# Performance work log

Measured on AMD Instinct MI355X. Metric: run time of the kernel, lower is better.

## Reference

```python
import jax, jax.numpy as jnp
import numpy as np

NEG_SLOPE = 0.2
EPS = 1e-5


def gatv2_conv(x, src, dst, Wl, Wr, att, bias, n_nodes):
    # x: [N, F_in]; Wl, Wr: [F_in, H*C]; att: [H, C]; bias: [C]
    H, C = att.shape
    xl = (x @ Wl).reshape(n_nodes, H, C)
    xr = (x @ Wr).reshape(n_nodes, H, C)
    # edge-wise GATv2 score: att . leaky_relu(xl[src] + xr[dst])
    xls = xl[src]                                   # [E, H, C]
    e = jax.nn.leaky_relu(xls + xr[dst], negative_slope=NEG_SLOPE)
    score = jnp.einsum('ehc,hc->eh', e, att)        # [E, H]
    # segment softmax over incoming edges of each dst node
    m = jax.ops.segment_max(score, dst, num_segments=n_nodes)
    expv = jnp.exp(score - m[dst])
    denom = jax.ops.segment_sum(expv, dst, num_segments=n_nodes)
    alpha = expv / denom[dst]                       # [E, H]
    out = jax.ops.segment_sum(xls * alpha[:, :, None], dst, num_segments=n_nodes)  # [N, H, C]
    return out.mean(axis=1) + bias                  # concat=False -> mean heads


def batchnorm(x, gamma, beta):
    mu = x.mean(axis=0)
    var = x.var(axis=0)
    return (x - mu) * jax.lax.rsqrt(var + EPS) * gamma + beta


def setup_inputs() -> dict:
    key = jax.random.key(0)
    ks = jax.random.split(key, 16)
    N, E = 50000, 400000
    F_in, Hd, H, Z = 32, 64, 4, 64

    def glorot(k, shape):
        fan_in, fan_out = shape[0], shape[-1]
        s = float(np.sqrt(6.0 / (fan_in + fan_out)))
        return jax.random.uniform(k, shape, jnp.float32, -s, s)

    return {
        'x': jax.random.normal(ks[0], (N, F_in), jnp.float32),
        'edge_index': jax.random.randint(ks[1], (2, E), 0, N, jnp.int64),
        'l': jax.random.uniform(ks[2], (N,), jnp.float32),
        'Wl1': glorot(ks[3], (F_in, H * Hd)),
        'Wr1': glorot(ks[4], (F_in, H * Hd)),
        'att1': glorot(ks[5], (H, Hd)),
        'b1': jnp.zeros((Hd,), jnp.float32),
        'g1': jnp.ones((Hd,), jnp.float32),
        'be1': jnp.zeros((Hd,), jnp.float32),
        'Wl2': glorot(ks[6], (Hd + 1, H * Hd)),
        'Wr2': glorot(ks[7], (Hd + 1, H * Hd)),
        'att2': glorot(ks[8], (H, Hd)),
        'b2': jnp.zeros((Hd,), jnp.float32),
        'g2': jnp.ones((Hd,), jnp.float32),
        'be2': jnp.zeros((Hd,), jnp.float32),
        'Wlin': glorot(ks[9], (Hd, 2 * Z)),
        'blin': jnp.zeros((2 * Z,), jnp.float32),
    }


def reference(x, edge_index, l, Wl1, Wr1, att1, b1, g1, be1,
              Wl2, Wr2, att2, b2, g2, be2, Wlin, blin):
    N = x.shape[0]
    loop = jnp.arange(N, dtype=edge_index.dtype)
    src = jnp.concatenate([edge_index[0], loop])  # add self-loops (PyG default)
    dst = jnp.concatenate([edge_index[1], loop])

    h = gatv2_conv(x, src, dst, Wl1, Wr1, att1, b1, N)
    h = jax.nn.relu(batchnorm(h, g1, be1))
    h = jnp.concatenate([h, l[:, None]], axis=-1)
    h = gatv2_conv(h, src, dst, Wl2, Wr2, att2, b2, N)
    h = jax.nn.relu(batchnorm(h, g2, be2))
    h = h @ Wlin + blin
    return h.mean(axis=0)  # [2*z_dim]
```

## Files before the change

kernel.cpp:

```cpp
#include <hip/hip_runtime.h>
#include <hip/hip_bf16.h>

typedef __hip_bfloat16 bf16;
typedef unsigned short u16;
typedef unsigned char u8;

#define NEG 0.2f
#define BN_EPS 1e-5f
#define SLOTS 64

typedef __attribute__((ext_vector_type(8))) short bfrag;
typedef __attribute__((ext_vector_type(4))) float ffrag;
typedef __attribute__((ext_vector_type(2))) float f32x2;

__device__ __forceinline__ float u2f(u16 u) { return __uint_as_float(((unsigned)u) << 16); }
__device__ __forceinline__ float lo2f(unsigned u) { return __uint_as_float(u << 16); }
__device__ __forceinline__ float hi2f(unsigned u) { return __uint_as_float(u & 0xffff0000u); }
__device__ __forceinline__ u16 f2b(float f) { bf16 t = __float2bfloat16(f); return *(u16*)&t; }
__device__ __forceinline__ float leaky(float x) { return fmaxf(x, NEG * x); }

__device__ __forceinline__ unsigned pk_fp8(float f0, float f1, float f2, float f3) {
    unsigned w = 0;
    w = __builtin_amdgcn_cvt_pk_fp8_f32(f0, f1, w, false);
    w = __builtin_amdgcn_cvt_pk_fp8_f32(f2, f3, w, true);
    return w;
}

__device__ __forceinline__ void prep_body(const float* __restrict__ Wl,
                                          const float* __restrict__ Wr,
                                          u16* __restrict__ Wbf, int K, int idx) {
    const int l = idx & 63, n = (idx >> 6) & 31, s = idx >> 11;
    const int col = n * 16 + (l & 15);
    const int kbase = s * 32 + ((l >> 4) << 3);
    const float* __restrict__ W = (col < 256) ? (Wl + col) : (Wr + col - 256);
    u16 v[8];
    #pragma unroll
    for (int j = 0; j < 8; ++j) {
        const int k = kbase + j;
        v[j] = (k < K) ? f2b(W[(size_t)k * 256]) : (u16)0;
    }
    ushort4* d = reinterpret_cast<ushort4*>(Wbf + (size_t)idx * 8);
    d[0] = make_ushort4(v[0], v[1], v[2], v[3]);
    d[1] = make_ushort4(v[4], v[5], v[6], v[7]);
}

__global__ __launch_bounds__(256) void k_misc(
    const float* __restrict__ Wl1, const float* __restrict__ Wr1,
    const float* __restrict__ Wl2, const float* __restrict__ Wr2,
    u16* __restrict__ WbfA, u16* __restrict__ WbfB,
    int* __restrict__ deg, int* __restrict__ scalars, int N) {
    const int b = blockIdx.x;
    if (b < 8) {
        prep_body(Wl1, Wr1, WbfA, 32, b * 256 + threadIdx.x);
    } else if (b < 32) {
        prep_body(Wl2, Wr2, WbfB, 65, (b - 8) * 256 + threadIdx.x);
    } else if (b == 32) {
        scalars[threadIdx.x] = 0;
        scalars[threadIdx.x + 256] = 0;
    } else {
        const int i = (b - 33) * 256 + (int)threadIdx.x;
        if (i < (N + 3) / 4)
            *reinterpret_cast<int4*>(deg + i * 4) = make_int4(0, 0, 0, 0);
    }
}

template <int KSTEPS, int STAGE>
__device__ __forceinline__ void gemm_body(
    int bid,
    const float* __restrict__ Xf,
    const u16* __restrict__ hagg,
    const float* __restrict__ sums, const float* __restrict__ sumsq,
    const float* __restrict__ g, const float* __restrict__ be,
    const float* __restrict__ lf,
    const u16* __restrict__ Wbf,
    u8* __restrict__ xl, u8* __restrict__ xr, int N) {

    __shared__ u16 sA[32 * 104];
    __shared__ u16 sC[32 * 512];
    __shared__ float ssc[64], ssh[64];

    const int tid = threadIdx.x;
    const int row0 = bid * 32;

    if (STAGE == 1) {
        if (tid < 64) {
            const float invN = 1.0f / (float)N;
            const float mu = sums[tid] * invN;
            const float var = sumsq[tid] * invN - mu * mu;
            const float sc = rsqrtf(var + BN_EPS) * g[tid];
            ssc[tid] = sc;
            ssh[tid] = be[tid] - mu * sc;
        }
        __syncthreads();
        for (int idx = tid; idx < 32 * 12; idx += 256) {
            const int r = idx / 12, c0 = (idx % 12) * 8;
            const int rr = row0 + r;
            u16 o[8] = {0, 0, 0, 0, 0, 0, 0, 0};
            if (rr < N) {
                if (c0 < 64) {
                    const uint4 hv = *reinterpret_cast<const uint4*>(hagg + (size_t)rr * 64 + c0);
                    const float f[8] = {lo2f(hv.x), hi2f(hv.x), lo2f(hv.y), hi2f(hv.y),
                                        lo2f(hv.z), hi2f(hv.z), lo2f(hv.w), hi2f(hv.w)};
                    #pragma unroll
                    for (int j = 0; j < 8; ++j)
                        o[j] = f2b(fmaxf(0.f, f[j] * ssc[c0 + j] + ssh[c0 + j]));
                } else if (c0 == 64) {
                    o[0] = f2b(lf[rr]);
                }
            }
            ushort4* d = reinterpret_cast<ushort4*>(&sA[r * 104 + c0]);
            d[0] = make_ushort4(o[0], o[1], o[2], o[3]);
            d[1] = make_ushort4(o[4], o[5], o[6], o[7]);
        }
    } else {
        for (int idx = tid; idx < 32 * 8; idx += 256) {
            const int r = idx >> 3, c4 = (idx & 7) * 4;
            const int rr = row0 + r;
            float4 v = make_float4(0.f, 0.f, 0.f, 0.f);
            if (rr < N) v = *reinterpret_cast<const float4*>(Xf + (size_t)rr * 32 + c4);
            *reinterpret_cast<ushort4*>(&sA[r * 104 + c4]) =
                make_ushort4(f2b(v.x), f2b(v.y), f2b(v.z), f2b(v.w));
        }
    }
    __syncthreads();

    const int w = tid >> 6, l = tid & 63;
    ffrag acc[2][8];
    #pragma unroll
    for (int m = 0; m < 2; ++m)
        #pragma unroll
        for (int n = 0; n < 8; ++n) acc[m][n] = ffrag{0.f, 0.f, 0.f, 0.f};

    #pragma unroll
    for (int s = 0; s < KSTEPS; ++s) {
        bfrag bf[8];
        #pragma unroll
        for (int n = 0; n < 8; ++n) {
            const int ntile = w * 8 + n;
            bf[n] = *reinterpret_cast<const bfrag*>(Wbf + ((size_t)(s * 32 + ntile) * 64 + l) * 8);
        }
        bfrag af[2];
        #pragma unroll
        for (int m = 0; m < 2; ++m) {
            const int off = (m * 16 + (l & 15)) * 104 + s * 32 + ((l >> 4) << 3);
            af[m] = *reinterpret_cast<const bfrag*>(&sA[off]);
        }
        #pragma unroll
        for (int n = 0; n < 8; ++n) {
            acc[0][n] = __builtin_amdgcn_mfma_f32_16x16x32_bf16(af[0], bf[n], acc[0][n], 0, 0, 0);
            acc[1][n] = __builtin_amdgcn_mfma_f32_16x16x32_bf16(af[1], bf[n], acc[1][n], 0, 0, 0);
        }
    }

    #pragma unroll
    for (int m = 0; m < 2; ++m)
        #pragma unroll
        for (int n = 0; n < 8; ++n) {
            const int col = w * 128 + n * 16 + (l & 15);
            const int rbase = m * 16 + ((l >> 4) << 2);
            #pragma unroll
            for (int j = 0; j < 4; ++j)
                sC[(rbase + j) * 512 + col] = f2b(acc[m][n][j]);
        }
    __syncthreads();

    for (int idx = tid; idx < 32 * 64; idx += 256) {
        const int r = idx >> 6, c8 = (idx & 63) * 8;
        const int rr = row0 + r;
        if (rr >= N) continue;
        const uint4 v = *reinterpret_cast<const uint4*>(&sC[r * 512 + c8]);
        uint2 o;
        o.x = pk_fp8(lo2f(v.x), hi2f(v.x), lo2f(v.y), hi2f(v.y));
        o.y = pk_fp8(lo2f(v.z), hi2f(v.z), lo2f(v.w), hi2f(v.w));
        if (c8 < 256)
            *reinterpret_cast<uint2*>(xl + (size_t)rr * 256 + c8) = o;
        else
            *reinterpret_cast<uint2*>(xr + (size_t)rr * 256 + (c8 - 256)) = o;
    }
}

__global__ __launch_bounds__(256) void k_gemm1_scatter(
    const float* __restrict__ Xf, const u16* __restrict__ WbfA,
    u8* __restrict__ xl, u8* __restrict__ xr, int N, int gemmBlocks,
    const int* __restrict__ src, const int* __restrict__ dst,
    int* __restrict__ deg, int* __restrict__ csr_off, int E) {
    if ((int)blockIdx.x < gemmBlocks) {
        gemm_body<1, 0>(blockIdx.x, Xf, nullptr, nullptr, nullptr, nullptr, nullptr,
                        nullptr, WbfA, xl, xr, N);
    } else {
        for (int e = ((int)blockIdx.x - gemmBlocks) * 256 + (int)threadIdx.x; e < E;
             e += 1024 * 256) {
            const int d = dst[e];
            const int slot = atomicAdd(&deg[d], 1);
            if (slot < SLOTS) csr_off[d * SLOTS + slot] = src[e] * 256;
        }
    }
}

__global__ __launch_bounds__(256) void k_gemm2(
    const u16* __restrict__ hagg,
    const float* __restrict__ sums, const float* __restrict__ sumsq,
    const float* __restrict__ g, const float* __restrict__ be,
    const float* __restrict__ lf, const u16* __restrict__ WbfB,
    u8* __restrict__ xl, u8* __restrict__ xr, int N) {
    gemm_body<3, 1>(blockIdx.x, nullptr, hagg, sums, sumsq, g, be, lf, WbfB, xl, xr, N);
}

__global__ __launch_bounds__(256) void gat_fused(
    const u8* __restrict__ xl, const u8* __restrict__ xr,
    const int* __restrict__ csr_off, const int* __restrict__ deg,
    const float* __restrict__ att,
    u16* __restrict__ hagg, int N) {
    const int tid = threadIdx.x;
    const int wv = tid >> 6, lane = tid & 63;
    const int id = blockIdx.x * 4 + wv;
    if (id >= N) return;
    const int half = lane >> 5, hl = lane & 31;

    const float4 av0 = *reinterpret_cast<const float4*>(att + hl * 8);
    const float4 av1 = *reinterpret_cast<const float4*>(att + hl * 8 + 4);
    const char* xlb = (const char*)xl;
    const unsigned selfOff = (unsigned)id * 256u;
    const unsigned laneOff = (unsigned)hl * 8u;

    const uint2 bu = *reinterpret_cast<const uint2*>((const char*)xr + selfOff + laneOff);
    const f32x2 bu01 = __builtin_amdgcn_cvt_pk_f32_fp8(bu.x, false);
    const f32x2 bu23 = __builtin_amdgcn_cvt_pk_f32_fp8(bu.x, true);
    const f32x2 bu45 = __builtin_amdgcn_cvt_pk_f32_fp8(bu.y, false);
    const f32x2 bu67 = __builtin_amdgcn_cvt_pk_f32_fp8(bu.y, true);
    const float b0 = bu01.x, b1 = bu01.y, b2 = bu23.x, b3 = bu23.y;
    const float b4 = bu45.x, b5 = bu45.y, b6 = bu67.x, b7 = bu67.y;

    const int L = min(deg[id], SLOTS);

    unsigned idxA = selfOff;
    if (lane < L) idxA = (unsigned)csr_off[id * SLOTS + lane];

    auto offv = [&](int vi) -> unsigned {
        const unsigned o = (unsigned)__shfl((int)idxA, vi - 1);
        return (vi == 0) ? selfOff : o;
    };
    auto ldrow = [&](int vi) -> uint2 {
        return *reinterpret_cast<const uint2*>(xlb + (size_t)(offv(vi) + laneOff));
    };

    float ax0 = 0.f, ax1 = 0.f, ax2 = 0.f, ax3 = 0.f;
    float ax4 = 0.f, ax5 = 0.f, ax6 = 0.f, ax7 = 0.f;
    float denom = 0.f;

    uint2 A = ldrow(half);
    uint2 B = ldrow(2 + half);

    #define PROC(a, vi)                                                         \
    {                                                                           \
        const f32x2 u01 = __builtin_amdgcn_cvt_pk_f32_fp8((a).x, false);        \
        const f32x2 u23 = __builtin_amdgcn_cvt_pk_f32_fp8((a).x, true);         \
        const f32x2 u45 = __builtin_amdgcn_cvt_pk_f32_fp8((a).y, false);        \
        const f32x2 u67 = __builtin_amdgcn_cvt_pk_f32_fp8((a).y, true);         \
        const float x0 = u01.x, x1 = u01.y, x2 = u23.x, x3 = u23.y;             \
        const float x4 = u45.x, x5 = u45.y, x6 = u67.x, x7 = u67.y;             \
        float p = av0.x * leaky(x0 + b0) + av0.y * leaky(x1 + b1)               \
                + av0.z * leaky(x2 + b2) + av0.w * leaky(x3 + b3)               \
                + av1.x * leaky(x4 + b4) + av1.y * leaky(x5 + b5)               \
                + av1.z * leaky(x6 + b6) + av1.w * leaky(x7 + b7);              \
        p += __shfl_xor(p, 1);                                                  \
        p += __shfl_xor(p, 2);                                                  \
        p += __shfl_xor(p, 4);                                                  \
        const float ev = ((vi) <= L) ? __expf(p) : 0.f;                         \
        denom += ev;                                                            \
        ax0 += ev * x0; ax1 += ev * x1; ax2 += ev * x2; ax3 += ev * x3;         \
        ax4 += ev * x4; ax5 += ev * x5; ax6 += ev * x6; ax7 += ev * x7;         \
    }

    for (int ib = 0; ib <= L; ib += 4) {
        uint2 An = A, Bn = B;
        if (ib + 4 <= L) An = ldrow(ib + 4 + half);
        if (ib + 6 <= L) Bn = ldrow(ib + 6 + half);
        PROC(A, ib + half)
        PROC(B, ib + 2 + half)
        A = An; B = Bn;
    }
    #undef PROC

    denom += __shfl_xor(denom, 32);
    const float s = 0.25f / denom;
    float r0 = ax0 * s, r1 = ax1 * s, r2 = ax2 * s, r3 = ax3 * s;
    float r4 = ax4 * s, r5 = ax5 * s, r6 = ax6 * s, r7 = ax7 * s;

    #define RED(r) r += __shfl_xor(r, 8); r += __shfl_xor(r, 16); r += __shfl_xor(r, 32);
    RED(r0) RED(r1) RED(r2) RED(r3) RED(r4) RED(r5) RED(r6) RED(r7)
    #undef RED

    if (lane < 8) {
        union { u16 h[8]; uint4 v; } pk;
        pk.h[0] = f2b(r0); pk.h[1] = f2b(r1); pk.h[2] = f2b(r2); pk.h[3] = f2b(r3);
        pk.h[4] = f2b(r4); pk.h[5] = f2b(r5); pk.h[6] = f2b(r6); pk.h[7] = f2b(r7);
        *reinterpret_cast<uint4*>(hagg + (size_t)id * 64 + lane * 8) = pk.v;
    }
}

__global__ __launch_bounds__(256) void bn_stats(const u16* __restrict__ hagg,
                                                float* __restrict__ sums,
                                                float* __restrict__ sumsq, int N) {
    __shared__ float bsum[64], bsq[64];
    const int tid = threadIdx.x;
    if (tid < 64) { bsum[tid] = 0.f; bsq[tid] = 0.f; }
    __syncthreads();
    const int r0 = tid >> 3, cg = tid & 7;
    float s[8] = {0, 0, 0, 0, 0, 0, 0, 0}, q[8] = {0, 0, 0, 0, 0, 0, 0, 0};
    for (int n = blockIdx.x * 32 + r0; n < N; n += gridDim.x * 32) {
        const uint4 v = *reinterpret_cast<const uint4*>(hagg + (size_t)n * 64 + cg * 8);
        const float f[8] = {lo2f(v.x), hi2f(v.x), lo2f(v.y), hi2f(v.y),
                            lo2f(v.z), hi2f(v.z), lo2f(v.w), hi2f(v.w)};
        #pragma unroll
        for (int j = 0; j < 8; ++j) { s[j] += f[j]; q[j] += f[j] * f[j]; }
    }
    #pragma unroll
    for (int j = 0; j < 8; ++j) {
        atomicAdd(&bsum[cg * 8 + j], s[j]);
        atomicAdd(&bsq[cg * 8 + j], q[j]);
    }
    __syncthreads();
    if (tid < 64) {
        atomicAdd(&sums[tid], bsum[tid]);
        atomicAdd(&sumsq[tid], bsq[tid]);
    }
}

__global__ __launch_bounds__(256) void bnz_final(
    const u16* __restrict__ hagg,
    const float* __restrict__ sums, const float* __restrict__ sumsq,
    const float* __restrict__ g, const float* __restrict__ be,
    const float* __restrict__ Wlin, const float* __restrict__ blin,
    float* __restrict__ zbar, int* __restrict__ counter,
    float* __restrict__ out, int N) {
    __shared__ float ls[4][64];
    __shared__ float zb[64];
    __shared__ int lastFlag;
    const int tid = threadIdx.x;
    const int c = tid & 63, r = tid >> 6;
    const float invN = 1.0f / (float)N;
    const float mu = sums[c] * invN;
    const float var = sumsq[c] * invN - mu * mu;
    const float sc = rsqrtf(var + BN_EPS) * g[c];
    const float sh = be[c] - mu * sc;
    float s = 0.f;
    for (int n = blockIdx.x * 4 + r; n < N; n += gridDim.x * 4)
        s += fmaxf(0.f, u2f(hagg[(size_t)n * 64 + c]) * sc + sh);
    ls[r][c] = s;
    __syncthreads();
    if (tid < 64) {
        atomicAdd(&zbar[tid], ls[0][tid] + ls[1][tid] + ls[2][tid] + ls[3][tid]);
        __threadfence();
    }
    __syncthreads();
    if (tid == 0) lastFlag = (atomicAdd(counter, 1) == (int)gridDim.x - 1) ? 1 : 0;
    __syncthreads();
    if (lastFlag) {
        if (tid < 64) zb[tid] = atomicAdd(&zbar[tid], 0.0f);
        __syncthreads();
        if (tid < 128) {
            float acc = blin[tid];
            #pragma unroll 4
            for (int k = 0; k < 64; ++k) acc += (zb[k] * invN) * Wlin[(size_t)k * 128 + tid];
            out[tid] = acc;
        }
    }
}

static inline char* align16(char* p) {
    return (char*)(((uintptr_t)p + 15) & ~(uintptr_t)15);
}

extern "C" void kernel_launch(void* const* d_in, const int* in_sizes, int n_in,
                              void* d_out, int out_size, void* d_ws, size_t ws_size,
                              hipStream_t stream) {
    const float* x    = (const float*)d_in[0];
    const int*   ei   = (const int*)d_in[1];
    const float* l    = (const float*)d_in[2];
    const float* Wl1  = (const float*)d_in[3];
    const float* Wr1  = (const float*)d_in[4];
    const float* att1 = (const float*)d_in[5];
    const float* g1   = (const float*)d_in[7];
    const float* be1  = (const float*)d_in[8];
    const float* Wl2  = (const float*)d_in[9];
    const float* Wr2  = (const float*)d_in[10];
    const float* att2 = (const float*)d_in[11];
    const float* g2   = (const float*)d_in[13];
    const float* be2  = (const float*)d_in[14];
    const float* Wlin = (const float*)d_in[15];
    const float* blin = (const float*)d_in[16];
    float* out = (float*)d_out;

    const int N = in_sizes[2];
    const int E = in_sizes[1] / 2;
    const int* src = ei;
    const int* dst = ei + E;

    char* p = (char*)d_ws;
    u8* xl = (u8*)p;            p += (size_t)N * 256 * sizeof(u8);
    u8* xr = (u8*)p;            p += (size_t)N * 256 * sizeof(u8);
    u16* hagg = (u16*)p;        p += (size_t)N * 64 * sizeof(u16);  p = align16(p);
    u16* WbfA = (u16*)p;        p += (size_t)2048 * 8 * sizeof(u16);
    u16* WbfB = (u16*)p;        p += (size_t)6144 * 8 * sizeof(u16);
    int* csr_off = (int*)p;     p += (size_t)N * SLOTS * sizeof(int);  p = align16(p);
    int* deg = (int*)p;         p += (size_t)((N + 3) / 4) * 4 * sizeof(int);  p = align16(p);
    int* scalars = (int*)p;
    float* sums1 = (float*)p;   p += 64 * sizeof(float);
    float* sumsq1 = (float*)p;  p += 64 * sizeof(float);
    float* sums2 = (float*)p;   p += 64 * sizeof(float);
    float* sumsq2 = (float*)p;  p += 64 * sizeof(float);
    float* zbar = (float*)p;    p += 64 * sizeof(float);
    int* counter = (int*)p;     p += 192 * sizeof(int);

    const int gemmBlocks = (N + 31) / 32;
    const int nodeBlocks = (N + 3) / 4;
    const int zeroBlocks = ((N + 3) / 4 + 255) / 256;

    k_misc<<<33 + zeroBlocks, 256, 0, stream>>>(Wl1, Wr1, Wl2, Wr2, WbfA, WbfB,
                                                deg, scalars, N);
    k_gemm1_scatter<<<gemmBlocks + 1024, 256, 0, stream>>>(x, WbfA, xl, xr, N, gemmBlocks,
                                                           src, dst, deg, csr_off, E);
    gat_fused<<<nodeBlocks, 256, 0, stream>>>(xl, xr, csr_off, deg, att1, hagg, N);
    bn_stats<<<256, 256, 0, stream>>>(hagg, sums1, sumsq1, N);
    k_gemm2<<<gemmBlocks, 256, 0, stream>>>(hagg, sums1, sumsq1, g1, be1, l, WbfB, xl, xr, N);
    gat_fused<<<nodeBlocks, 256, 0, stream>>>(xl, xr, csr_off, deg, att2, hagg, N);
    bn_stats<<<256, 256, 0, stream>>>(hagg, sums2, sumsq2, N);
    bnz_final<<<256, 256, 0, stream>>>(hagg, sums2, sumsq2, g2, be2, Wlin, blin,
                                       zbar, counter, out, N);
}
```

Before: 198.0 us.

## Move edge scatter into prep kernel, memset zeroing, convert GEMM output to fp8 in registers

Zeroing of the degree and scalar buffers now uses one hipMemsetAsync. The CSR edge scatter moves out of the GEMM1 kernel into the weight-prep kernel, so GEMM1 runs as its own kernel. The GEMM epilogue converts accumulators straight to fp8 before writing to shared memory, which halves the staging buffer and drops the bf16 round-trip; the copy-out then uses 16-byte stores. GEMM1 also uses a narrower shared A tile. The byte-wise shared stores may cause bank conflicts, and the fp8 values are now rounded once from fp32 instead of through bf16.

```diff
diff --git a/kernel.cpp b/kernel.cpp
--- a/kernel.cpp
+++ b/kernel.cpp
@@ -18,13 +18,6 @@
 __device__ __forceinline__ float hi2f(unsigned u) { return __uint_as_float(u & 0xffff0000u); }
 __device__ __forceinline__ u16 f2b(float f) { bf16 t = __float2bfloat16(f); return *(u16*)&t; }
 __device__ __forceinline__ float leaky(float x) { return fmaxf(x, NEG * x); }
-
-__device__ __forceinline__ unsigned pk_fp8(float f0, float f1, float f2, float f3) {
-    unsigned w = 0;
-    w = __builtin_amdgcn_cvt_pk_fp8_f32(f0, f1, w, false);
-    w = __builtin_amdgcn_cvt_pk_fp8_f32(f2, f3, w, true);
-    return w;
-}
 
 __device__ __forceinline__ void prep_body(const float* __restrict__ Wl,
                                           const float* __restrict__ Wr,
@@ -48,23 +41,23 @@
     const float* __restrict__ Wl1, const float* __restrict__ Wr1,
     const float* __restrict__ Wl2, const float* __restrict__ Wr2,
     u16* __restrict__ WbfA, u16* __restrict__ WbfB,
-    int* __restrict__ deg, int* __restrict__ scalars, int N) {
+    const int* __restrict__ src, const int* __restrict__ dst,
+    int* __restrict__ deg, int* __restrict__ csr_off, int E) {
     const int b = blockIdx.x;
     if (b < 8) {
         prep_body(Wl1, Wr1, WbfA, 32, b * 256 + threadIdx.x);
     } else if (b < 32) {
         prep_body(Wl2, Wr2, WbfB, 65, (b - 8) * 256 + threadIdx.x);
-    } else if (b == 32) {
-        scalars[threadIdx.x] = 0;
-        scalars[threadIdx.x + 256] = 0;
     } else {
-        const int i = (b - 33) * 256 + (int)threadIdx.x;
-        if (i < (N + 3) / 4)
-            *reinterpret_cast<int4*>(deg + i * 4) = make_int4(0, 0, 0, 0);
-    }
-}
-
-template <int KSTEPS, int STAGE>
+        for (int e = (b - 32) * 256 + (int)threadIdx.x; e < E; e += 1024 * 256) {
+            const int d = dst[e];
+            const int slot = atomicAdd(&deg[d], 1);
+            if (slot < SLOTS) csr_off[d * SLOTS + slot] = src[e] * 256;
+        }
+    }
+}
+
+template <int KSTEPS, int STAGE, int SAW>
 __device__ __forceinline__ void gemm_body(
     int bid,
     const float* __restrict__ Xf,
@@ -75,8 +68,8 @@
     const u16* __restrict__ Wbf,
     u8* __restrict__ xl, u8* __restrict__ xr, int N) {
 
-    __shared__ u16 sA[32 * 104];
-    __shared__ u16 sC[32 * 512];
+    __shared__ u16 sA[32 * SAW];
+    __shared__ u8 sC[32 * 512];
     __shared__ float ssc[64], ssh[64];
 
     const int tid = threadIdx.x;
@@ -108,7 +101,7 @@
                     o[0] = f2b(lf[rr]);
                 }
             }
-            ushort4* d = reinterpret_cast<ushort4*>(&sA[r * 104 + c0]);
+            ushort4* d = reinterpret_cast<ushort4*>(&sA[r * SAW + c0]);
             d[0] = make_ushort4(o[0], o[1], o[2], o[3]);
             d[1] = make_ushort4(o[4], o[5], o[6], o[7]);
         }
@@ -118,7 +111,7 @@
             const int rr = row0 + r;
             float4 v = make_float4(0.f, 0.f, 0.f, 0.f);
             if (rr < N) v = *reinterpret_cast<const float4*>(Xf + (size_t)rr * 32 + c4);
-            *reinterpret_cast<ushort4*>(&sA[r * 104 + c4]) =
+            *reinterpret_cast<ushort4*>(&sA[r * SAW + c4]) =
                 make_ushort4(f2b(v.x), f2b(v.y), f2b(v.z), f2b(v.w));
         }
     }
@@ -142,7 +135,7 @@
         bfrag af[2];
         #pragma unroll
         for (int m = 0; m < 2; ++m) {
-            const int off = (m * 16 + (l & 15)) * 104 + s * 32 + ((l >> 4) << 3);
+            const int off = (m * 16 + (l & 15)) * SAW + s * 32 + ((l >> 4) << 3);
             af[m] = *reinterpret_cast<const bfrag*>(&sA[off]);
         }
         #pragma unroll
@@ -158,43 +151,32 @@
         for (int n = 0; n < 8; ++n) {
             const int col = w * 128 + n * 16 + (l & 15);
             const int rbase = m * 16 + ((l >> 4) << 2);
-            #pragma unroll
-            for (int j = 0; j < 4; ++j)
-                sC[(rbase + j) * 512 + col] = f2b(acc[m][n][j]);
-        }
-    __syncthreads();
-
-    for (int idx = tid; idx < 32 * 64; idx += 256) {
-        const int r = idx >> 6, c8 = (idx & 63) * 8;
+            unsigned w01 = __builtin_amdgcn_cvt_pk_fp8_f32(acc[m][n][0], acc[m][n][1], 0u, false);
+            unsigned w23 = __builtin_amdgcn_cvt_pk_fp8_f32(acc[m][n][2], acc[m][n][3], 0u, false);
+            sC[(rbase + 0) * 512 + col] = (u8)(w01 & 0xff);
+            sC[(rbase + 1) * 512 + col] = (u8)((w01 >> 8) & 0xff);
+            sC[(rbase + 2) * 512 + col] = (u8)(w23 & 0xff);
+            sC[(rbase + 3) * 512 + col] = (u8)((w23 >> 8) & 0xff);
+        }
+    __syncthreads();
+
+    for (int idx = tid; idx < 32 * 32; idx += 256) {
+        const int r = idx >> 5, c16 = (idx & 31) * 16;
         const int rr = row0 + r;
         if (rr >= N) continue;
-        const uint4 v = *reinterpret_cast<const uint4*>(&sC[r * 512 + c8]);
-        uint2 o;
-        o.x = pk_fp8(lo2f(v.x), hi2f(v.x), lo2f(v.y), hi2f(v.y));
-        o.y = pk_fp8(lo2f(v.z), hi2f(v.z), lo2f(v.w), hi2f(v.w));
-        if (c8 < 256)
-            *reinterpret_cast<uint2*>(xl + (size_t)rr * 256 + c8) = o;
+        const uint4 v = *reinterpret_cast<const uint4*>(&sC[r * 512 + c16]);
+        if (c16 < 256)
+            *reinterpret_cast<uint4*>(xl + (size_t)rr * 256 + c16) = v;
         else
-            *reinterpret_cast<uint2*>(xr + (size_t)rr * 256 + (c8 - 256)) = o;
-    }
-}
-
-__global__ __launch_bounds__(256) void k_gemm1_scatter(
+            *reinterpret_cast<uint4*>(xr + (size_t)rr * 256 + (c16 - 256)) = v;
+    }
+}
+
+__global__ __launch_bounds__(256) void k_gemm1(
     const float* __restrict__ Xf, const u16* __restrict__ WbfA,
-    u8* __restrict__ xl, u8* __restrict__ xr, int N, int gemmBlocks,
-    const int* __restrict__ src, const int* __restrict__ dst,
-    int* __restrict__ deg, int* __restrict__ csr_off, int E) {
-    if ((int)blockIdx.x < gemmBlocks) {
-        gemm_body<1, 0>(blockIdx.x, Xf, nullptr, nullptr, nullptr, nullptr, nullptr,
+    u8* __restrict__ xl, u8* __restrict__ xr, int N) {
+    gemm_body<1, 0, 40>(blockIdx.x, Xf, nullptr, nullptr, nullptr, nullptr, nullptr,
                         nullptr, WbfA, xl, xr, N);
-    } else {
-        for (int e = ((int)blockIdx.x - gemmBlocks) * 256 + (int)threadIdx.x; e < E;
-             e += 1024 * 256) {
-            const int d = dst[e];
-            const int slot = atomicAdd(&deg[d], 1);
-            if (slot < SLOTS) csr_off[d * SLOTS + slot] = src[e] * 256;
-        }
-    }
 }
 
 __global__ __launch_bounds__(256) void k_gemm2(
@@ -203,7 +185,7 @@
     const float* __restrict__ g, const float* __restrict__ be,
     const float* __restrict__ lf, const u16* __restrict__ WbfB,
     u8* __restrict__ xl, u8* __restrict__ xr, int N) {
-    gemm_body<3, 1>(blockIdx.x, nullptr, hagg, sums, sumsq, g, be, lf, WbfB, xl, xr, N);
+    gemm_body<3, 1, 104>(blockIdx.x, nullptr, hagg, sums, sumsq, g, be, lf, WbfB, xl, xr, N);
 }
 
 __global__ __launch_bounds__(256) void gat_fused(
@@ -404,7 +386,8 @@
     u16* WbfA = (u16*)p;        p += (size_t)2048 * 8 * sizeof(u16);
     u16* WbfB = (u16*)p;        p += (size_t)6144 * 8 * sizeof(u16);
     int* csr_off = (int*)p;     p += (size_t)N * SLOTS * sizeof(int);  p = align16(p);
-    int* deg = (int*)p;         p += (size_t)((N + 3) / 4) * 4 * sizeof(int);  p = align16(p);
+    char* zero0 = p;
+    int* deg = (int*)p;         p += (size_t)N * sizeof(int);
     int* scalars = (int*)p;
     float* sums1 = (float*)p;   p += 64 * sizeof(float);
     float* sumsq1 = (float*)p;  p += 64 * sizeof(float);
@@ -412,15 +395,16 @@
     float* sumsq2 = (float*)p;  p += 64 * sizeof(float);
     float* zbar = (float*)p;    p += 64 * sizeof(float);
     int* counter = (int*)p;     p += 192 * sizeof(int);
+    const size_t zbytes = (size_t)(p - zero0);
+    (void)scalars;
 
     const int gemmBlocks = (N + 31) / 32;
     const int nodeBlocks = (N + 3) / 4;
-    const int zeroBlocks = ((N + 3) / 4 + 255) / 256;
-
-    k_misc<<<33 + zeroBlocks, 256, 0, stream>>>(Wl1, Wr1, Wl2, Wr2, WbfA, WbfB,
-                                                deg, scalars, N);
-    k_gemm1_scatter<<<gemmBlocks + 1024, 256, 0, stream>>>(x, WbfA, xl, xr, N, gemmBlocks,
-                                                           src, dst, deg, csr_off, E);
+
+    hipMemsetAsync(zero0, 0, zbytes, stream);
+    k_misc<<<32 + 1024, 256, 0, stream>>>(Wl1, Wr1, Wl2, Wr2, WbfA, WbfB,
+                                          src, dst, deg, csr_off, E);
+    k_gemm1<<<gemmBlocks, 256, 0, stream>>>(x, WbfA, xl, xr, N);
     gat_fused<<<nodeBlocks, 256, 0, stream>>>(xl, xr, csr_off, deg, att1, hagg, N);
     bn_stats<<<256, 256, 0, stream>>>(hagg, sums1, sumsq1, N);
     k_gemm2<<<gemmBlocks, 256, 0, stream>>>(hagg, sums1, sumsq1, g1, be1, l, WbfB, xl, xr, N);
```

Result: faster. 188.2 us (-4.9%).
